# Kernel optimization log

Hardware: AMD Instinct MI355X
Metric: run time of the kernel (lower is better)

Reference implementation:

```python
import jax, jax.numpy as jnp
import numpy as np

NEG_SLOPE = 0.01  # F.leaky_relu default
BN_EPS = 1e-5


def leaky(v):
    return jnp.where(v > 0, v, NEG_SLOPE * v)


def mesh_conv(x, gemm_edges, W):
    # x: [B, C, E, 1] -> squeeze; gemm_edges: [B, E, 4] int; W: [O, C, 7]
    x = x[..., 0]                                   # [B, C, E]
    B, C, E = x.shape
    xp = jnp.concatenate([jnp.zeros((B, C, 1), x.dtype), x], axis=2)  # pad slot 0
    eid = jnp.broadcast_to(jnp.arange(E, dtype=gemm_edges.dtype)[None, :, None], (B, E, 1))
    gi = jnp.concatenate([eid, gemm_edges], axis=2) + 1               # [B, E, 5]
    # gather: f[b, c, e, j] = xp[b, c, gi[b, e, j]]
    f = jax.vmap(lambda xb, ib: xb[:, ib])(xp, gi)                    # [B, C, E, 5]
    f0, f1, f2, f3, f4 = (f[..., i] for i in range(5))
    x1 = f1 + f3
    x2 = f2 + f4
    x3 = jnp.abs(f1 - f3)
    x4 = jnp.abs(f2 - f4)
    x5 = f1 + f2 + f3 + f4
    avg = x5 / 4
    x6 = (f1 - avg) ** 2 + (f2 - avg) ** 2 + (f3 - avg) ** 2 + (f4 - avg) ** 2
    G = jnp.stack([f0, x1, x2, x3, x4, x5, x6], axis=3)               # [B, C, E, 7]
    out = jnp.einsum('bcek,ock->boe', G, W)                           # conv2d (1,k), no bias
    return out[..., None]                                             # [B, O, E, 1]


def batchnorm(h, gamma, beta):
    # training-mode BatchNorm2d over dims (B, E, 1) per channel
    mean = jnp.mean(h, axis=(0, 2, 3), keepdims=True)
    var = jnp.mean((h - mean) ** 2, axis=(0, 2, 3), keepdims=True)
    hn = (h - mean) * jax.lax.rsqrt(var + BN_EPS)
    return hn * gamma[None, :, None, None] + beta[None, :, None, None]


def setup_inputs() -> dict:
    key = jax.random.key(0)
    ks = jax.random.split(key, 6)
    B, Cin, Cout, E, K, SKIPS = 4, 128, 256, 16384, 7, 3
    x = jax.random.normal(ks[0], (B, Cin, E, 1), dtype=jnp.float32)
    gemm_edges = jax.random.randint(ks[1], (B, E, 4), 0, E, dtype=jnp.int32)
    W0 = jax.random.normal(ks[2], (Cout, Cin, K), dtype=jnp.float32) * (1.0 / np.sqrt(Cin * K))
    Ws = jax.random.normal(ks[3], (SKIPS, Cout, Cout, K), dtype=jnp.float32) * (1.0 / np.sqrt(Cout * K))
    gammas = jnp.ones((SKIPS, Cout), dtype=jnp.float32)
    betas = jnp.zeros((SKIPS, Cout), dtype=jnp.float32)
    return {"x": x, "gemm_edges": gemm_edges, "W0": W0, "Ws": Ws,
            "gammas": gammas, "betas": betas}


def reference(x, gemm_edges, W0, Ws, gammas, betas):
    h = mesh_conv(x, gemm_edges, W0)
    h1 = h
    for i in range(Ws.shape[0]):  # fixed small skips loop
        h = batchnorm(leaky(h), gammas[i], betas[i])
        h = mesh_conv(h, gemm_edges, Ws[i])
    h = h + h1
    return leaky(h)
```

## Files before the change

### kernel.cpp

```cpp
#include <hip/hip_runtime.h>
#include <hip/hip_bf16.h>


#define B_ 4
#define E_ 16384

typedef short short8 __attribute__((ext_vector_type(8)));
typedef float floatx4 __attribute__((ext_vector_type(4)));

__device__ __forceinline__ float lk(float v) { return v > 0.0f ? v : 0.01f * v; }
__device__ __forceinline__ float b2f(__hip_bfloat16 h) { return __bfloat162float(h); }
__device__ __forceinline__ __hip_bfloat16 f2b(float f) { return __float2bfloat16(f); }

__device__ __forceinline__ void barrier_lds() {
    __builtin_amdgcn_fence(__ATOMIC_RELEASE, "workgroup", "local");
    __builtin_amdgcn_s_barrier();
    __builtin_amdgcn_fence(__ATOMIC_ACQUIRE, "workgroup", "local");
}

template <typename TS>
struct Cvt;
template <>
struct Cvt<float> {
    static __device__ __forceinline__ float to(float f) { return f; }
    static __device__ __forceinline__ float from(float s) { return s; }
    static __device__ __forceinline__ float ld1(const float* p) { return *p; }
};
template <>
struct Cvt<__hip_bfloat16> {
    static __device__ __forceinline__ __hip_bfloat16 to(float f) { return f2b(f); }
    static __device__ __forceinline__ float from(__hip_bfloat16 s) { return b2f(s); }
    static __device__ __forceinline__ float ld1(const __hip_bfloat16* p) { return b2f(*p); }
};

template <typename TS>
__global__ void k_transpose_x(const float* __restrict__ x, TS* __restrict__ xT) {
    __shared__ float t[32][33];
    const int b = blockIdx.z, c0 = blockIdx.y * 32, e0 = blockIdx.x * 32;
    const int tx = threadIdx.x & 31, ty = threadIdx.x >> 5;
#pragma unroll
    for (int i = 0; i < 4; ++i) {
        const int c = ty + i * 8;
        t[c][tx] = x[((size_t)b * 128 + c0 + c) * E_ + e0 + tx];
    }
    __syncthreads();
#pragma unroll
    for (int i = 0; i < 4; ++i) {
        const int e = ty + i * 8;
        xT[((size_t)b * E_ + e0 + e) * 128 + c0 + tx] = Cvt<TS>::to(t[tx][e]);
    }
}

__global__ void k_prep_w(const float* __restrict__ w, __hip_bfloat16* __restrict__ wf2, int C) {
    const int NCH = C / 8;
    const int idx = blockIdx.x * blockDim.x + threadIdx.x;
    const int lane = idx & 63, t = idx >> 6;
    const int ks = t & 1, nt = (t >> 1) & 3, w4 = (t >> 3) & 3, ci = t >> 5;
    if (ci >= NCH) return;
    const int o = w4 * 64 + nt * 16 + (lane & 15);
    const int c = ci * 8 + ks * 4 + (lane >> 4);
    const float* src = w + ((size_t)o * C + c) * 7;
    __hip_bfloat16* dst = wf2 + (size_t)idx * 8;
#pragma unroll
    for (int f = 0; f < 7; ++f) dst[f] = f2b(src[f]);
    dst[7] = f2b(0.0f);
}

__global__ void k_bn_finalize(const float* __restrict__ stats, const float* __restrict__ gamma,
                              const float* __restrict__ beta, float* __restrict__ scale,
                              float* __restrict__ bias) {
    const int c = threadIdx.x;
    const float n = 1.0f / 65536.0f;
    const float mean = stats[c] * n;
    const float var = stats[256 + c] * n - mean * mean;
    const float inv = rsqrtf(var + 1e-5f);
    const float s = gamma[c] * inv;
    scale[c] = s;
    bias[c] = beta[c] - mean * s;
}

template <int C, bool BN, bool STATS, bool FINAL, typename TS>
__global__ __launch_bounds__(512, 4) void k_conv(const TS* __restrict__ hin,
                                                 const int* __restrict__ edges,
                                                 const __hip_bfloat16* __restrict__ wf2,
                                                 const float* __restrict__ scale,
                                                 const float* __restrict__ bias,
                                                 TS* __restrict__ hout,
                                                 float* __restrict__ stats,
                                                 const TS* __restrict__ h1res,
                                                 float* __restrict__ outf) {
    constexpr int NCH = C / 8;
    constexpr int ASA = 72;
    __shared__ __align__(16) __hip_bfloat16 Asm[2][64 * ASA];
    __shared__ float ssc[256];
    __shared__ float ssb[256];
    __shared__ float ssum[STATS ? 256 : 1];
    __shared__ float ssq[STATS ? 256 : 1];

    const int tid = threadIdx.x;
    const int tm = blockIdx.x;
    const int b = tm >> 8;
    const int e0 = (tm & 255) * 64;
    const int wave = tid >> 6, lane = tid & 63;

    if constexpr (BN) {
        if (tid < C) {
            ssc[tid] = scale[tid];
            ssb[tid] = bias[tid];
        }
    }
    if constexpr (STATS) {
        if (tid < 256) {
            ssum[tid] = 0.0f;
            ssq[tid] = 0.0f;
        }
    }

    const int e_loc = tid >> 3;
    const int ch = tid & 7;
    const TS* rp0;
    const TS* rp1;
    const TS* rp2;
    const TS* rp3;
    const TS* rp4;
    {
        const int4 nb =
            *reinterpret_cast<const int4*>(edges + (((size_t)b * E_) + e0 + e_loc) * 4);
        const size_t rb = (size_t)b * E_;
        rp0 = hin + (rb + e0 + e_loc) * C + ch;
        rp1 = hin + (rb + nb.x) * C + ch;
        rp2 = hin + (rb + nb.y) * C + ch;
        rp3 = hin + (rb + nb.z) * C + ch;
        rp4 = hin + (rb + nb.w) * C + ch;
    }

    floatx4 acc[2][4];
#pragma unroll
    for (int i = 0; i < 2; ++i)
#pragma unroll
        for (int j = 0; j < 4; ++j) {
            floatx4 z = {0.0f, 0.0f, 0.0f, 0.0f};
            acc[i][j] = z;
        }

    const int wm = (wave & 1) * 32;
    const int w4 = wave >> 1;
    const int wn = w4 * 64;
    const int qd = lane >> 4, l15 = lane & 15;

    float pf[5];
    auto issue_gathers = [&](int cch) {
        const int co = cch * 8;
        pf[0] = Cvt<TS>::ld1(rp0 + co);
        pf[1] = Cvt<TS>::ld1(rp1 + co);
        pf[2] = Cvt<TS>::ld1(rp2 + co);
        pf[3] = Cvt<TS>::ld1(rp3 + co);
        pf[4] = Cvt<TS>::ld1(rp4 + co);
    };
    auto produce = [&](int cch, int bs) {
        float f0 = pf[0], f1 = pf[1], f2 = pf[2], f3 = pf[3], f4 = pf[4];
        if constexpr (BN) {
            const float sA = ssc[cch * 8 + ch];
            const float bA = ssb[cch * 8 + ch];
            f0 = lk(f0) * sA + bA;
            f1 = lk(f1) * sA + bA;
            f2 = lk(f2) * sA + bA;
            f3 = lk(f3) * sA + bA;
            f4 = lk(f4) * sA + bA;
        }
        float gf[8];
        gf[0] = f0;
        gf[1] = f1 + f3;
        gf[2] = f2 + f4;
        gf[3] = fabsf(f1 - f3);
        gf[4] = fabsf(f2 - f4);
        gf[5] = gf[1] + gf[2];
        const float avg = 0.25f * gf[5];
        const float d1 = f1 - avg, d2 = f2 - avg, d3 = f3 - avg, d4 = f4 - avg;
        gf[6] = d1 * d1 + d2 * d2 + d3 * d3 + d4 * d4;
        gf[7] = 0.0f;
        union U {
            short8 v;
            __hip_bfloat16 h[8];
        } uh;
#pragma unroll
        for (int f = 0; f < 8; ++f) uh.h[f] = f2b(gf[f]);
        *reinterpret_cast<short8*>(&Asm[bs][e_loc * ASA + ch * 8]) = uh.v;
    };

    short8 bq[2][4];

    issue_gathers(0);
#pragma unroll
    for (int ks = 0; ks < 2; ++ks)
#pragma unroll
        for (int nt = 0; nt < 4; ++nt)
            bq[ks][nt] = *reinterpret_cast<const short8*>(
                wf2 + ((((size_t)0 * 4 + w4) * 4 + nt) * 2 + ks) * 512 + lane * 8);
    if constexpr (BN) barrier_lds();
    produce(0, 0);
    issue_gathers(1);
    barrier_lds();

    for (int ci = 0; ci < NCH; ++ci) {
        const int cur = ci & 1;

        if (ci + 1 < NCH) {
            produce(ci + 1, cur ^ 1);
            if (ci + 2 < NCH) issue_gathers(ci + 2);
        }

        __builtin_amdgcn_s_setprio(1);
#pragma unroll
        for (int ks = 0; ks < 2; ++ks) {
#pragma unroll
            for (int mt = 0; mt < 2; ++mt) {
                const int r = (wm + mt * 16 + l15) * ASA + ks * 32 + qd * 8;
                const short8 ah = *reinterpret_cast<const short8*>(&Asm[cur][r]);
#pragma unroll
                for (int nt = 0; nt < 4; ++nt)
                    acc[mt][nt] = __builtin_amdgcn_mfma_f32_16x16x32_bf16(ah, bq[ks][nt],
                                                                          acc[mt][nt], 0, 0, 0);
            }
        }
        __builtin_amdgcn_s_setprio(0);

        if (ci + 1 < NCH) {
#pragma unroll
            for (int ks = 0; ks < 2; ++ks)
#pragma unroll
                for (int nt = 0; nt < 4; ++nt)
                    bq[ks][nt] = *reinterpret_cast<const short8*>(
                        wf2 + ((((size_t)(ci + 1) * 4 + w4) * 4 + nt) * 2 + ks) * 512 +
                        lane * 8);
        }

        barrier_lds();
    }

    const size_t orow0 = (size_t)b * E_ + e0;
    float snt[4], qnt[4];
    if constexpr (STATS) {
#pragma unroll
        for (int nt = 0; nt < 4; ++nt) {
            snt[nt] = 0.0f;
            qnt[nt] = 0.0f;
        }
    }
#pragma unroll
    for (int mt = 0; mt < 2; ++mt) {
#pragma unroll
        for (int nt = 0; nt < 4; ++nt) {
            const int col = wn + nt * 16 + l15;
            const size_t r0 = orow0 + wm + mt * 16 + qd * 4;
            if constexpr (FINAL) {
                float4 o4;
                o4.x = lk(acc[mt][nt][0] + Cvt<TS>::from(h1res[(r0 + 0) * 256 + col]));
                o4.y = lk(acc[mt][nt][1] + Cvt<TS>::from(h1res[(r0 + 1) * 256 + col]));
                o4.z = lk(acc[mt][nt][2] + Cvt<TS>::from(h1res[(r0 + 2) * 256 + col]));
                o4.w = lk(acc[mt][nt][3] + Cvt<TS>::from(h1res[(r0 + 3) * 256 + col]));
                const int erow = e0 + wm + mt * 16 + qd * 4;
                *reinterpret_cast<float4*>(&outf[((size_t)b * 256 + col) * E_ + erow]) = o4;
            } else {
#pragma unroll
                for (int r = 0; r < 4; ++r) {
                    const float v = acc[mt][nt][r];
                    hout[(r0 + r) * 256 + col] = Cvt<TS>::to(v);
                    if constexpr (STATS) {
                        const float lv = lk(v);
                        snt[nt] += lv;
                        qnt[nt] += lv * lv;
                    }
                }
            }
        }
    }
    if constexpr (STATS) {
#pragma unroll
        for (int nt = 0; nt < 4; ++nt) {
            atomicAdd(&ssum[wn + nt * 16 + l15], snt[nt]);
            atomicAdd(&ssq[wn + nt * 16 + l15], qnt[nt]);
        }
        __syncthreads();
        if (tid < 256) {
            atomicAdd(&stats[tid], ssum[tid]);
            atomicAdd(&stats[256 + tid], ssq[tid]);
        }
    }
}

template <typename TS>
static void run_all(const float* x, const int* edges, const float* W0, const float* Ws,
                    const float* gammas, const float* betas, float* out, char* ws,
                    hipStream_t stream) {
    const size_t hbytes = (size_t)B_ * E_ * 256 * sizeof(TS);
    TS* h1 = (TS*)(ws);
    TS* hA = (TS*)(ws + hbytes);
    TS* hB = (TS*)(ws + 2 * hbytes);
    TS* xT = (TS*)(ws + 2 * hbytes);
    char* wp = ws + 3 * hbytes;
    __hip_bfloat16* wf0 = (__hip_bfloat16*)(wp);
    __hip_bfloat16* wfs[3];
    for (int i = 0; i < 3; ++i)
        wfs[i] = (__hip_bfloat16*)(wp + (512u << 10) + (size_t)i * (1u << 20));
    float* stats = (float*)(wp + (4u << 20));
    float* scale = (float*)(wp + (4u << 20) + 8192);
    float* bias = (float*)(wp + (4u << 20) + 9216);

    hipMemsetAsync(stats, 0, 3 * 512 * sizeof(float), stream);
    k_transpose_x<TS><<<dim3(E_ / 32, 4, B_), 256, 0, stream>>>(x, xT);
    k_prep_w<<<128, 256, 0, stream>>>(W0, wf0, 128);
    for (int i = 0; i < 3; ++i)
        k_prep_w<<<256, 256, 0, stream>>>(Ws + (size_t)i * 458752, wfs[i], 256);

    const dim3 gconv(1024);
    k_conv<128, false, true, false, TS><<<gconv, 512, 0, stream>>>(
        xT, edges, wf0, nullptr, nullptr, h1, stats, nullptr, nullptr);

    TS* bin[3] = {h1, hA, hB};
    TS* bout[3] = {hA, hB, nullptr};
    for (int i = 0; i < 3; ++i) {
        k_bn_finalize<<<1, 256, 0, stream>>>(stats + 512 * i, gammas + 256 * i, betas + 256 * i,
                                             scale, bias);
        if (i < 2) {
            k_conv<256, true, true, false, TS><<<gconv, 512, 0, stream>>>(
                bin[i], edges, wfs[i], scale, bias, bout[i], stats + 512 * (i + 1), nullptr,
                nullptr);
        } else {
            k_conv<256, true, false, true, TS><<<gconv, 512, 0, stream>>>(
                bin[i], edges, wfs[i], scale, bias, nullptr, nullptr, h1, out);
        }
    }
}

extern "C" void kernel_launch(void* const* d_in, const int* in_sizes, int n_in, void* d_out,
                              int out_size, void* d_ws, size_t ws_size, hipStream_t stream) {
    const float* x = (const float*)d_in[0];
    const int* edges = (const int*)d_in[1];
    const float* W0 = (const float*)d_in[2];
    const float* Ws = (const float*)d_in[3];
    const float* gammas = (const float*)d_in[4];
    const float* betas = (const float*)d_in[5];
    float* out = (float*)d_out;
    char* ws = (char*)d_ws;

    if (ws_size >= 208670720ULL + 4096ULL)
        run_all<float>(x, edges, W0, Ws, gammas, betas, out, ws, stream);
    else
        run_all<__hip_bfloat16>(x, edges, W0, Ws, gammas, betas, out, ws, stream);
}
```

Baseline: 604.9 us.

## Process two channel chunks per LDS stage and pre-reduce stats with shuffles

The main loop now handles 16 input channels per stage instead of 8, so each stage holds two chunks in LDS with a wider row stride. This halves the number of block barriers. Gathers for two chunks are issued together, and the produce step for the next stage is placed between the two MFMA halves to overlap feature computation with matrix math. The BN-stat accumulation also reduces across quads with shuffles before the LDS atomics, cutting atomic traffic, at the cost of more LDS and more registers per thread.

```diff
diff --git a/kernel.cpp b/kernel.cpp
--- a/kernel.cpp
+++ b/kernel.cpp
@@ -89,8 +89,8 @@
                                                  float* __restrict__ stats,
                                                  const TS* __restrict__ h1res,
                                                  float* __restrict__ outf) {
-    constexpr int NCH = C / 8;
-    constexpr int ASA = 72;
+    constexpr int NST = C / 16;
+    constexpr int ASA = 136;
     __shared__ __align__(16) __hip_bfloat16 Asm[2][64 * ASA];
     __shared__ float ssc[256];
     __shared__ float ssb[256];
@@ -148,44 +148,53 @@
     const int wn = w4 * 64;
     const int qd = lane >> 4, l15 = lane & 15;
 
-    float pf[5];
-    auto issue_gathers = [&](int cch) {
-        const int co = cch * 8;
-        pf[0] = Cvt<TS>::ld1(rp0 + co);
-        pf[1] = Cvt<TS>::ld1(rp1 + co);
-        pf[2] = Cvt<TS>::ld1(rp2 + co);
-        pf[3] = Cvt<TS>::ld1(rp3 + co);
-        pf[4] = Cvt<TS>::ld1(rp4 + co);
+    float pf[5][2];
+    auto issue_gathers = [&](int ss) {
+        const int co = ss * 16;
+        pf[0][0] = Cvt<TS>::ld1(rp0 + co);
+        pf[1][0] = Cvt<TS>::ld1(rp1 + co);
+        pf[2][0] = Cvt<TS>::ld1(rp2 + co);
+        pf[3][0] = Cvt<TS>::ld1(rp3 + co);
+        pf[4][0] = Cvt<TS>::ld1(rp4 + co);
+        pf[0][1] = Cvt<TS>::ld1(rp0 + co + 8);
+        pf[1][1] = Cvt<TS>::ld1(rp1 + co + 8);
+        pf[2][1] = Cvt<TS>::ld1(rp2 + co + 8);
+        pf[3][1] = Cvt<TS>::ld1(rp3 + co + 8);
+        pf[4][1] = Cvt<TS>::ld1(rp4 + co + 8);
     };
-    auto produce = [&](int cch, int bs) {
-        float f0 = pf[0], f1 = pf[1], f2 = pf[2], f3 = pf[3], f4 = pf[4];
-        if constexpr (BN) {
-            const float sA = ssc[cch * 8 + ch];
-            const float bA = ssb[cch * 8 + ch];
-            f0 = lk(f0) * sA + bA;
-            f1 = lk(f1) * sA + bA;
-            f2 = lk(f2) * sA + bA;
-            f3 = lk(f3) * sA + bA;
-            f4 = lk(f4) * sA + bA;
-        }
-        float gf[8];
-        gf[0] = f0;
-        gf[1] = f1 + f3;
-        gf[2] = f2 + f4;
-        gf[3] = fabsf(f1 - f3);
-        gf[4] = fabsf(f2 - f4);
-        gf[5] = gf[1] + gf[2];
-        const float avg = 0.25f * gf[5];
-        const float d1 = f1 - avg, d2 = f2 - avg, d3 = f3 - avg, d4 = f4 - avg;
-        gf[6] = d1 * d1 + d2 * d2 + d3 * d3 + d4 * d4;
-        gf[7] = 0.0f;
-        union U {
-            short8 v;
-            __hip_bfloat16 h[8];
-        } uh;
-#pragma unroll
-        for (int f = 0; f < 8; ++f) uh.h[f] = f2b(gf[f]);
-        *reinterpret_cast<short8*>(&Asm[bs][e_loc * ASA + ch * 8]) = uh.v;
+    auto produce = [&](int ss, int bs) {
+#pragma unroll
+        for (int s2 = 0; s2 < 2; ++s2) {
+            float f0 = pf[0][s2], f1 = pf[1][s2], f2 = pf[2][s2], f3 = pf[3][s2],
+                  f4 = pf[4][s2];
+            if constexpr (BN) {
+                const float sA = ssc[ss * 16 + s2 * 8 + ch];
+                const float bA = ssb[ss * 16 + s2 * 8 + ch];
+                f0 = lk(f0) * sA + bA;
+                f1 = lk(f1) * sA + bA;
+                f2 = lk(f2) * sA + bA;
+                f3 = lk(f3) * sA + bA;
+                f4 = lk(f4) * sA + bA;
+            }
+            float gf[8];
+            gf[0] = f0;
+            gf[1] = f1 + f3;
+            gf[2] = f2 + f4;
+            gf[3] = fabsf(f1 - f3);
+            gf[4] = fabsf(f2 - f4);
+            gf[5] = gf[1] + gf[2];
+            const float avg = 0.25f * gf[5];
+            const float d1 = f1 - avg, d2 = f2 - avg, d3 = f3 - avg, d4 = f4 - avg;
+            gf[6] = d1 * d1 + d2 * d2 + d3 * d3 + d4 * d4;
+            gf[7] = 0.0f;
+            union U {
+                short8 v;
+                __hip_bfloat16 h[8];
+            } uh;
+#pragma unroll
+            for (int f = 0; f < 8; ++f) uh.h[f] = f2b(gf[f]);
+            *reinterpret_cast<short8*>(&Asm[bs][e_loc * ASA + (s2 * 8 + ch) * 8]) = uh.v;
+        }
     };
 
     short8 bq[2][4];
@@ -202,13 +211,8 @@
     issue_gathers(1);
     barrier_lds();
 
-    for (int ci = 0; ci < NCH; ++ci) {
-        const int cur = ci & 1;
-
-        if (ci + 1 < NCH) {
-            produce(ci + 1, cur ^ 1);
-            if (ci + 2 < NCH) issue_gathers(ci + 2);
-        }
+    for (int ss = 0; ss < NST; ++ss) {
+        const int cur = ss & 1;
 
         __builtin_amdgcn_s_setprio(1);
 #pragma unroll
@@ -225,14 +229,42 @@
         }
         __builtin_amdgcn_s_setprio(0);
 
-        if (ci + 1 < NCH) {
+        {
+            const size_t ci = 2 * (size_t)ss + 1;
 #pragma unroll
             for (int ks = 0; ks < 2; ++ks)
 #pragma unroll
                 for (int nt = 0; nt < 4; ++nt)
                     bq[ks][nt] = *reinterpret_cast<const short8*>(
-                        wf2 + ((((size_t)(ci + 1) * 4 + w4) * 4 + nt) * 2 + ks) * 512 +
-                        lane * 8);
+                        wf2 + (((ci * 4 + w4) * 4 + nt) * 2 + ks) * 512 + lane * 8);
+        }
+
+        if (ss + 1 < NST) produce(ss + 1, cur ^ 1);
+
+        __builtin_amdgcn_s_setprio(1);
+#pragma unroll
+        for (int ks = 0; ks < 2; ++ks) {
+#pragma unroll
+            for (int mt = 0; mt < 2; ++mt) {
+                const int r = (wm + mt * 16 + l15) * ASA + (ks + 2) * 32 + qd * 8;
+                const short8 ah = *reinterpret_cast<const short8*>(&Asm[cur][r]);
+#pragma unroll
+                for (int nt = 0; nt < 4; ++nt)
+                    acc[mt][nt] = __builtin_amdgcn_mfma_f32_16x16x32_bf16(ah, bq[ks][nt],
+                                                                          acc[mt][nt], 0, 0, 0);
+            }
+        }
+        __builtin_amdgcn_s_setprio(0);
+
+        if (ss + 1 < NST) {
+            const size_t ci = 2 * (size_t)(ss + 1);
+#pragma unroll
+            for (int ks = 0; ks < 2; ++ks)
+#pragma unroll
+                for (int nt = 0; nt < 4; ++nt)
+                    bq[ks][nt] = *reinterpret_cast<const short8*>(
+                        wf2 + (((ci * 4 + w4) * 4 + nt) * 2 + ks) * 512 + lane * 8);
+            if (ss + 2 < NST) issue_gathers(ss + 2);
         }
 
         barrier_lds();
@@ -278,8 +310,15 @@
     if constexpr (STATS) {
 #pragma unroll
         for (int nt = 0; nt < 4; ++nt) {
-            atomicAdd(&ssum[wn + nt * 16 + l15], snt[nt]);
-            atomicAdd(&ssq[wn + nt * 16 + l15], qnt[nt]);
+            float s = snt[nt], q = qnt[nt];
+            s += __shfl_xor(s, 16);
+            q += __shfl_xor(q, 16);
+            s += __shfl_xor(s, 32);
+            q += __shfl_xor(q, 32);
+            if (qd == 0) {
+                atomicAdd(&ssum[wn + nt * 16 + l15], s);
+                atomicAdd(&ssq[wn + nt * 16 + l15], q);
+            }
         }
         __syncthreads();
         if (tid < 256) {
```

Result: faster. 511.5 us, median of 3 (-15.4%).
